# Kernel optimization log

Measured on AMD Instinct MI355X. Metric: run time of the kernel, lower is better.

## Reference

```python
import jax, jax.numpy as jnp
import numpy as np

B, S = 2, 2048
HQ, HKV, D = 32, 8, 128
SCALING = 0.08838834764831845  # 1/sqrt(128)
E4M3_MAX = 448.0
FP4_MAX = 6.0
# e2m1 representable magnitudes and decision midpoints
FP4_GRID = jnp.array([0.0, 0.5, 1.0, 1.5, 2.0, 3.0, 4.0, 6.0], dtype=jnp.float32)
FP4_MID = (FP4_GRID[:-1] + FP4_GRID[1:]) / 2.0


def quant_dequant_e4m3(x):
    """Simulate torch .to(float8_e4m3fn): clamp to +-448, round mantissa to 3 bits."""
    ax = jnp.abs(x)
    xc = jnp.clip(x, -E4M3_MAX, E4M3_MAX)
    e = jnp.clip(jnp.floor(jnp.log2(jnp.maximum(ax, 1e-12))), -6.0, 8.0)
    q = jnp.round(xc * jnp.exp2(3.0 - e)) * jnp.exp2(e - 3.0)
    return jnp.where(ax == 0.0, 0.0, q)


def quant_dequant_fp4(x):
    """FP4 (e2m1) compress/decompress with per-(token,head) absmax scale over head_dim.
    x: [B, S, H, D] -> dequantized [B, S, H, D]."""
    scale = jnp.max(jnp.abs(x), axis=-1, keepdims=True) / FP4_MAX  # [B,S,H,1]
    scale = jnp.maximum(scale, 1e-12)
    xn = x / scale
    idx = jnp.searchsorted(FP4_MID, jnp.abs(xn))  # nearest e2m1 magnitude
    return jnp.sign(xn) * FP4_GRID[idx] * scale


def setup_inputs() -> dict:
    key = jax.random.key(0)
    kq, kk, kv = jax.random.split(key, 3)
    q = jax.random.normal(kq, (B, S, HQ * D), dtype=jnp.float32)
    k = jax.random.normal(kk, (B, S, HKV * D), dtype=jnp.float32)
    v = jax.random.normal(kv, (B, S, HKV * D), dtype=jnp.float32)
    return {"q": q, "k": k, "v": v}


def reference(q, k, v):
    # reshape to heads
    qh = q.reshape(B, S, HQ, D)
    kh = k.reshape(B, S, HKV, D)
    vh = v.reshape(B, S, HKV, D)
    # FP8 cast then FP4 compress/decompress of the KV cache
    kq8 = quant_dequant_e4m3(kh)
    vq8 = quant_dequant_e4m3(vh)
    kd = quant_dequant_fp4(kq8)
    vd = quant_dequant_fp4(vq8)
    # GQA: expand kv heads to query heads
    g = HQ // HKV
    kr = jnp.repeat(kd, g, axis=2)  # [B,S,HQ,D]
    vr = jnp.repeat(vd, g, axis=2)
    scores = jnp.einsum("bqhd,bkhd->bhqk", qh, kr) * SCALING  # [B,HQ,S,S]
    causal = jnp.tril(jnp.ones((S, S), dtype=bool))
    scores = jnp.where(causal[None, None], scores, jnp.float32(-1e30))
    probs = jax.nn.softmax(scores, axis=-1)
    out = jnp.einsum("bhqk,bkhd->bqhd", probs, vr)
    return out.reshape(B, S, HQ * D)
```

## Files before the change

### kernel.cpp

```cpp
#include <hip/hip_runtime.h>
#include <cstdint>
#include <cstddef>

#define B_    2
#define S_    2048
#define HQ_   32
#define HKV_  8
#define D_    128
#define QSCALE_ (0.08838834764831845f * 1.4426950408889634f)

#define NROW_ (B_*S_*HKV_)

typedef __bf16 bf16x8 __attribute__((ext_vector_type(8)));
typedef float  f32x4  __attribute__((ext_vector_type(4)));

__device__ __forceinline__ unsigned short f2bfu(float f) {
    __bf16 b = (__bf16)f;
    return __builtin_bit_cast(unsigned short, b);
}

__device__ __forceinline__ void gl_lds16(const unsigned short* g, unsigned short* l) {
    __builtin_amdgcn_global_load_lds(
        (const __attribute__((address_space(1))) void*)g,
        (__attribute__((address_space(3))) void*)l, 16, 0, 0);
}

__device__ __forceinline__ float qd_e4m3(float x) {
    float ax = fabsf(x);
    float xc = fminf(fmaxf(x, -448.f), 448.f);
    float axc = fmaxf(ax, 1e-12f);
    int e = (int)((__builtin_bit_cast(unsigned int, axc) >> 23) & 255u) - 127;
    e = min(max(e, -6), 8);
    float s1 = __builtin_bit_cast(float, (unsigned int)(130 - e) << 23);
    float s2 = __builtin_bit_cast(float, (unsigned int)(124 + e) << 23);
    float q = rintf(xc * s1) * s2;
    return ax == 0.f ? 0.f : q;
}

__device__ __forceinline__ float qd_fp4(float x, float scale) {
    float xn = x / scale;
    float a = fabsf(xn);
    float g;
    if      (a <= 0.25f) g = 0.f;
    else if (a <= 0.75f) g = 0.5f;
    else if (a <= 1.25f) g = 1.f;
    else if (a <= 1.75f) g = 1.5f;
    else if (a <= 2.5f)  g = 2.f;
    else if (a <= 3.5f)  g = 3.f;
    else if (a <= 5.f)   g = 4.f;
    else                 g = 6.f;
    return copysignf(g * scale, xn);
}

__global__ __launch_bounds__(256) void quant_kv(const float* __restrict__ k,
                                                const float* __restrict__ v,
                                                unsigned short* __restrict__ kd,
                                                unsigned short* __restrict__ vd) {
    int gw = (blockIdx.x * 256 + threadIdx.x) >> 6;
    int lane = threadIdx.x & 63;
    int row = gw;
    const float* src;
    unsigned short* dst;
    if (row < NROW_) { src = k; dst = kd; }
    else             { row -= NROW_; src = v; dst = vd; }
    int b   = row / (S_ * HKV_);
    int rem = row - b * (S_ * HKV_);
    int s   = rem >> 3;
    int h   = rem & 7;
    float2 x = *(const float2*)(src + (size_t)row * D_ + 2 * lane);
    float q0 = qd_e4m3(x.x);
    float q1 = qd_e4m3(x.y);
    float amax = fmaxf(fabsf(q0), fabsf(q1));
#pragma unroll
    for (int m = 1; m < 64; m <<= 1) amax = fmaxf(amax, __shfl_xor(amax, m, 64));
    float scale = fmaxf(amax / 6.0f, 1e-12f);
    float y0 = qd_fp4(q0, scale);
    float y1 = qd_fp4(q1, scale);
    size_t outOff = ((size_t)(b * HKV_ + h) * S_ + s) * D_ + 2 * lane;
    unsigned int pack = (unsigned int)f2bfu(y0) | ((unsigned int)f2bfu(y1) << 16);
    *(unsigned int*)(dst + outOff) = pack;
}

__global__ __launch_bounds__(256) void transpose_v(const unsigned short* __restrict__ vd,
                                                   unsigned short* __restrict__ vdT) {
    __shared__ alignas(16) unsigned short t[64][136];
    int bh = blockIdx.x >> 5;
    int st = blockIdx.x & 31;
    int s0 = st * 64;
    int tid = threadIdx.x;
    {
        int row = tid >> 2;
        const unsigned short* sp = vd + ((size_t)bh * S_ + s0 + row) * D_;
#pragma unroll
        for (int i = 0; i < 4; ++i) {
            int c = (tid & 3) + 4 * i;
            *(uint4*)&t[row][c * 8] = *(const uint4*)(sp + c * 8);
        }
    }
    __syncthreads();
    {
        int d = tid >> 1;
        unsigned short* dp = vdT + ((size_t)bh * D_ + d) * S_ + s0;
#pragma unroll
        for (int i = 0; i < 4; ++i) {
            int c = (tid & 1) + 2 * i;
            int so = c * 8;
            unsigned short tmp[8];
#pragma unroll
            for (int e = 0; e < 8; ++e) tmp[e] = t[so + e][d];
            *(uint4*)(dp + so) = *(uint4*)tmp;
        }
    }
}

__global__ __launch_bounds__(256) void attn(const float* __restrict__ q,
                                            const unsigned short* __restrict__ kd,
                                            const unsigned short* __restrict__ vdT,
                                            float* __restrict__ out) {
    int bh = blockIdx.x;
    int yp = blockIdx.y;
    int b  = bh >> 5;
    int hq = bh & 31;
    int hkv = hq >> 2;
    int tid  = threadIdx.x;
    int lane = tid & 63;
    int wave = tid >> 6;
    int m16  = lane & 15;
    int g    = lane >> 4;
    int m8   = m16 & 7;

    __shared__ alignas(16) unsigned short ks[64 * 128];
    __shared__ alignas(16) unsigned short vs[128 * 64];
    __shared__ alignas(16) unsigned short ps[4 * 16 * 64];

    const unsigned short* kbase = kd  + (size_t)(b * HKV_ + hkv) * S_ * D_;
    const unsigned short* vbase = vdT + (size_t)(b * HKV_ + hkv) * D_ * S_;

    bf16x8 vones;
#pragma unroll
    for (int j = 0; j < 8; ++j) vones[j] = (__bf16)1.0f;

    for (int phase = 0; phase < 2; ++phase) {
        int qt = phase ? yp : (31 - yp);
        int q0 = qt * 64;
        int qrowBase = q0 + wave * 16;

        bf16x8 qf[4];
        const float* qp = q + (((size_t)b * S_ + (qrowBase + m16)) * HQ_ + hq) * D_;
#pragma unroll
        for (int c = 0; c < 4; ++c) {
            const float* p0 = qp + c * 32 + g * 8;
            bf16x8 f;
#pragma unroll
            for (int j = 0; j < 8; ++j) f[j] = (__bf16)(p0[j] * QSCALE_);
            qf[c] = f;
        }

        f32x4 o[8];
#pragma unroll
        for (int i = 0; i < 8; ++i) o[i] = (f32x4){0.f, 0.f, 0.f, 0.f};
        f32x4 o9 = (f32x4){0.f, 0.f, 0.f, 0.f};

        for (int kt = 0; kt <= qt; ++kt) {
            int k0 = kt * 64;
            __syncthreads();
#pragma unroll
            for (int i = 0; i < 4; ++i) {
                int row = wave * 16 + i * 4 + (lane >> 4);
                int c = (lane & 15) ^ (row & 15);
                gl_lds16(kbase + (size_t)(k0 + row) * D_ + c * 8,
                         &ks[wave * 2048 + i * 512]);
            }
#pragma unroll
            for (int i = 0; i < 4; ++i) {
                int d = wave * 32 + i * 8 + (lane >> 3);
                int c = (lane & 7) ^ (d & 7);
                gl_lds16(vbase + (size_t)d * S_ + k0 + c * 8,
                         &vs[wave * 2048 + i * 512]);
            }
            __syncthreads();

            bool diag = (kt == qt);
            int kcmax = diag ? ((wave >> 1) + 1) : 2;

            f32x4 sacc[4];
#pragma unroll
            for (int n = 0; n < 4; ++n) sacc[n] = (f32x4){0.f, 0.f, 0.f, 0.f};
#pragma unroll
            for (int n = 0; n < 4; ++n) {
                if (!diag || n <= wave) {
#pragma unroll
                    for (int c = 0; c < 4; ++c) {
                        bf16x8 ak = *(const bf16x8*)&ks[(n * 16 + m16) * 128 +
                                                        (((c * 4 + g) ^ m16) * 8)];
                        sacc[n] = __builtin_amdgcn_mfma_f32_16x16x32_bf16(ak, qf[c], sacc[n], 0, 0, 0);
                    }
                }
            }

            int qloc = wave * 16 + m16;
            float pv[4][4];
#pragma unroll
            for (int n = 0; n < 4; ++n) {
                if (!diag || n <= wave) {
#pragma unroll
                    for (int r = 0; r < 4; ++r) {
                        float p = exp2f(sacc[n][r]);
                        if (diag) {
                            int key = n * 16 + g * 4 + r;
                            p = (key <= qloc) ? p : 0.f;
                        }
                        pv[n][r] = p;
                    }
                }
            }

#pragma unroll
            for (int n = 0; n < 4; ++n) {
                if (n < 2 * kcmax) {
                    unsigned int lo = 0, hi = 0;
                    if (!diag || n <= wave) {
                        lo = (unsigned int)f2bfu(pv[n][0]) | ((unsigned int)f2bfu(pv[n][1]) << 16);
                        hi = (unsigned int)f2bfu(pv[n][2]) | ((unsigned int)f2bfu(pv[n][3]) << 16);
                    }
                    int chunk = (n * 2 + (g >> 1)) ^ m8;
                    uint2 val; val.x = lo; val.y = hi;
                    *(uint2*)&ps[wave * 1024 + m16 * 64 + chunk * 8 + (g & 1) * 4] = val;
                }
            }
            asm volatile("s_waitcnt lgkmcnt(0)" ::: "memory");

#pragma unroll
            for (int kc = 0; kc < 2; ++kc) {
                if (kc < kcmax) {
                    bf16x8 pa = *(const bf16x8*)&ps[wave * 1024 + m16 * 64 +
                                                    (((kc * 4 + g) ^ m8) * 8)];
                    o9 = __builtin_amdgcn_mfma_f32_16x16x32_bf16(pa, vones, o9, 0, 0, 0);
#pragma unroll
                    for (int ds = 0; ds < 8; ++ds) {
                        bf16x8 vb = *(const bf16x8*)&vs[(ds * 16 + m16) * 64 +
                                                        (((kc * 4 + g) ^ m8) * 8)];
                        o[ds] = __builtin_amdgcn_mfma_f32_16x16x32_bf16(pa, vb, o[ds], 0, 0, 0);
                    }
                }
            }
        }

#pragma unroll
        for (int r = 0; r < 4; ++r) {
            float inv = 1.f / o9[r];
            float* op = out + (((size_t)b * S_ + (qrowBase + g * 4 + r)) * HQ_ + hq) * D_;
#pragma unroll
            for (int ds = 0; ds < 8; ++ds)
                op[ds * 16 + m16] = o[ds][r] * inv;
        }
    }
}

extern "C" void kernel_launch(void* const* d_in, const int* in_sizes, int n_in,
                              void* d_out, int out_size, void* d_ws, size_t ws_size,
                              hipStream_t stream) {
    const float* q = (const float*)d_in[0];
    const float* k = (const float*)d_in[1];
    const float* v = (const float*)d_in[2];
    float* out = (float*)d_out;

    unsigned short* kd  = (unsigned short*)d_ws;
    unsigned short* vd  = kd + (size_t)NROW_ * D_;
    unsigned short* vdT = vd + (size_t)NROW_ * D_;

    quant_kv<<<16384, 256, 0, stream>>>(k, v, kd, vd);
    transpose_v<<<512, 256, 0, stream>>>(vd, vdT);
    attn<<<dim3(64, 16), 256, 0, stream>>>(q, kd, vdT, out);
}
```

Before: 260.3 us.

## Double-buffer K/V tiles and process 128-row query tiles with two fragments per wave

```diff
diff --git a/kernel.cpp b/kernel.cpp
--- a/kernel.cpp
+++ b/kernel.cpp
@@ -113,10 +113,10 @@
     }
 }
 
-__global__ __launch_bounds__(256) void attn(const float* __restrict__ q,
-                                            const unsigned short* __restrict__ kd,
-                                            const unsigned short* __restrict__ vdT,
-                                            float* __restrict__ out) {
+__global__ __launch_bounds__(256, 2) void attn(const float* __restrict__ q,
+                                               const unsigned short* __restrict__ kd,
+                                               const unsigned short* __restrict__ vdT,
+                                               float* __restrict__ out) {
     int bh = blockIdx.x;
     int yp = blockIdx.y;
     int b  = bh >> 5;
@@ -129,9 +129,9 @@
     int g    = lane >> 4;
     int m8   = m16 & 7;
 
-    __shared__ alignas(16) unsigned short ks[64 * 128];
-    __shared__ alignas(16) unsigned short vs[128 * 64];
-    __shared__ alignas(16) unsigned short ps[4 * 16 * 64];
+    __shared__ alignas(16) unsigned short ks[2][64 * 128];
+    __shared__ alignas(16) unsigned short vs[2][128 * 64];
+    __shared__ alignas(16) unsigned short ps[4 * 2048];
 
     const unsigned short* kbase = kd  + (size_t)(b * HKV_ + hkv) * S_ * D_;
     const unsigned short* vbase = vdT + (size_t)(b * HKV_ + hkv) * D_ * S_;
@@ -140,119 +140,181 @@
 #pragma unroll
     for (int j = 0; j < 8; ++j) vones[j] = (__bf16)1.0f;
 
+    auto stage = [&](int buf, int k0s) {
+#pragma unroll
+        for (int i = 0; i < 4; ++i) {
+            int row = wave * 16 + i * 4 + (lane >> 4);
+            int c = (lane & 15) ^ (row & 15);
+            gl_lds16(kbase + (size_t)(k0s + row) * D_ + c * 8,
+                     &ks[buf][wave * 2048 + i * 512]);
+        }
+#pragma unroll
+        for (int i = 0; i < 4; ++i) {
+            int d = wave * 32 + i * 8 + (lane >> 3);
+            int c = (lane & 7) ^ (d & 7);
+            gl_lds16(vbase + (size_t)d * S_ + k0s + c * 8,
+                     &vs[buf][wave * 2048 + i * 512]);
+        }
+    };
+
     for (int phase = 0; phase < 2; ++phase) {
-        int qt = phase ? yp : (31 - yp);
-        int q0 = qt * 64;
-        int qrowBase = q0 + wave * 16;
-
-        bf16x8 qf[4];
-        const float* qp = q + (((size_t)b * S_ + (qrowBase + m16)) * HQ_ + hq) * D_;
-#pragma unroll
-        for (int c = 0; c < 4; ++c) {
-            const float* p0 = qp + c * 32 + g * 8;
-            bf16x8 f;
-#pragma unroll
-            for (int j = 0; j < 8; ++j) f[j] = (__bf16)(p0[j] * QSCALE_);
-            qf[c] = f;
-        }
-
-        f32x4 o[8];
-#pragma unroll
-        for (int i = 0; i < 8; ++i) o[i] = (f32x4){0.f, 0.f, 0.f, 0.f};
-        f32x4 o9 = (f32x4){0.f, 0.f, 0.f, 0.f};
-
-        for (int kt = 0; kt <= qt; ++kt) {
+        int t  = phase ? yp : (15 - yp);
+        int q0 = t * 128;
+        int nkt = 2 * t + 2;
+
+        stage(0, 0);
+
+        bf16x8 qf0[4], qf1[4];
+        {
+            const float* qp0 = q + (((size_t)b * S_ + (q0 + wave * 32 + m16)) * HQ_ + hq) * D_;
+            const float* qp1 = qp0 + (size_t)16 * HQ_ * D_;
+#pragma unroll
+            for (int c = 0; c < 4; ++c) {
+                const float* a0 = qp0 + c * 32 + g * 8;
+                const float* a1 = qp1 + c * 32 + g * 8;
+                bf16x8 f0, f1;
+#pragma unroll
+                for (int j = 0; j < 8; ++j) {
+                    f0[j] = (__bf16)(a0[j] * QSCALE_);
+                    f1[j] = (__bf16)(a1[j] * QSCALE_);
+                }
+                qf0[c] = f0;
+                qf1[c] = f1;
+            }
+        }
+
+        f32x4 o0[8], o1[8];
+#pragma unroll
+        for (int i = 0; i < 8; ++i) { o0[i] = (f32x4){0.f,0.f,0.f,0.f}; o1[i] = (f32x4){0.f,0.f,0.f,0.f}; }
+        f32x4 l0 = (f32x4){0.f,0.f,0.f,0.f};
+        f32x4 l1 = (f32x4){0.f,0.f,0.f,0.f};
+
+        __syncthreads();
+
+        int cur = 0;
+        for (int kt = 0; kt < nkt; ++kt) {
             int k0 = kt * 64;
-            __syncthreads();
-#pragma unroll
-            for (int i = 0; i < 4; ++i) {
-                int row = wave * 16 + i * 4 + (lane >> 4);
-                int c = (lane & 15) ^ (row & 15);
-                gl_lds16(kbase + (size_t)(k0 + row) * D_ + c * 8,
-                         &ks[wave * 2048 + i * 512]);
-            }
-#pragma unroll
-            for (int i = 0; i < 4; ++i) {
-                int d = wave * 32 + i * 8 + (lane >> 3);
-                int c = (lane & 7) ^ (d & 7);
-                gl_lds16(vbase + (size_t)d * S_ + k0 + c * 8,
-                         &vs[wave * 2048 + i * 512]);
+            if (kt + 1 < nkt) stage(cur ^ 1, k0 + 64);
+
+            int base1 = (q0 - k0) + wave * 32 + 16;
+            if (base1 >= 0) {
+                int base0 = base1 - 16;
+                bool full1 = base1 >= 64, full0 = base0 >= 64;
+                int a1 = full1 ? 4 : (base1 >> 4) + 1;
+                int a0 = (base0 < 0) ? 0 : (full0 ? 4 : (base0 >> 4) + 1);
+                int kcm1 = (a1 + 1) >> 1;
+                int kcm0 = (a0 + 1) >> 1;
+
+                f32x4 s0[4], s1[4];
+#pragma unroll
+                for (int n = 0; n < 4; ++n) {
+                    s0[n] = (f32x4){0.f,0.f,0.f,0.f};
+                    s1[n] = (f32x4){0.f,0.f,0.f,0.f};
+                }
+#pragma unroll
+                for (int n = 0; n < 4; ++n) {
+                    if (n < a1) {
+#pragma unroll
+                        for (int c = 0; c < 4; ++c) {
+                            bf16x8 ak = *(const bf16x8*)&ks[cur][(n * 16 + m16) * 128 +
+                                                                 (((c * 4 + g) ^ m16) * 8)];
+                            s1[n] = __builtin_amdgcn_mfma_f32_16x16x32_bf16(ak, qf1[c], s1[n], 0, 0, 0);
+                            if (n < a0)
+                                s0[n] = __builtin_amdgcn_mfma_f32_16x16x32_bf16(ak, qf0[c], s0[n], 0, 0, 0);
+                        }
+                    }
+                }
+
+#pragma unroll
+                for (int n = 0; n < 4; ++n) {
+                    if (n < 2 * kcm1) {
+                        unsigned int lo = 0, hi = 0;
+                        if (n < a1) {
+                            float pr[4];
+#pragma unroll
+                            for (int r = 0; r < 4; ++r) {
+                                float p = exp2f(s1[n][r]);
+                                if (!full1) {
+                                    int key = n * 16 + g * 4 + r;
+                                    p = (key <= base1 + m16) ? p : 0.f;
+                                }
+                                pr[r] = p;
+                            }
+                            lo = (unsigned int)f2bfu(pr[0]) | ((unsigned int)f2bfu(pr[1]) << 16);
+                            hi = (unsigned int)f2bfu(pr[2]) | ((unsigned int)f2bfu(pr[3]) << 16);
+                        }
+                        int chunk = (n * 2 + (g >> 1)) ^ m8;
+                        uint2 val; val.x = lo; val.y = hi;
+                        *(uint2*)&ps[wave * 2048 + 1024 + m16 * 64 + chunk * 8 + (g & 1) * 4] = val;
+                    }
+                }
+                if (a0 > 0) {
+#pragma unroll
+                    for (int n = 0; n < 4; ++n) {
+                        if (n < 2 * kcm0) {
+                            unsigned int lo = 0, hi = 0;
+                            if (n < a0) {
+                                float pr[4];
+#pragma unroll
+                                for (int r = 0; r < 4; ++r) {
+                                    float p = exp2f(s0[n][r]);
+                                    if (!full0) {
+                                        int key = n * 16 + g * 4 + r;
+                                        p = (key <= base0 + m16) ? p : 0.f;
+                                    }
+                                    pr[r] = p;
+                                }
+                                lo = (unsigned int)f2bfu(pr[0]) | ((unsigned int)f2bfu(pr[1]) << 16);
+                                hi = (unsigned int)f2bfu(pr[2]) | ((unsigned int)f2bfu(pr[3]) << 16);
+                            }
+                            int chunk = (n * 2 + (g >> 1)) ^ m8;
+                            uint2 val; val.x = lo; val.y = hi;
+                            *(uint2*)&ps[wave * 2048 + m16 * 64 + chunk * 8 + (g & 1) * 4] = val;
+                        }
+                    }
+                }
+                asm volatile("s_waitcnt lgkmcnt(0)" ::: "memory");
+
+#pragma unroll
+                for (int kc = 0; kc < 2; ++kc) {
+                    if (kc < kcm1) {
+                        bf16x8 pa1 = *(const bf16x8*)&ps[wave * 2048 + 1024 + m16 * 64 +
+                                                         (((kc * 4 + g) ^ m8) * 8)];
+                        l1 = __builtin_amdgcn_mfma_f32_16x16x32_bf16(pa1, vones, l1, 0, 0, 0);
+                        bool use0 = kc < kcm0;
+                        bf16x8 pa0;
+                        if (use0) {
+                            pa0 = *(const bf16x8*)&ps[wave * 2048 + m16 * 64 +
+                                                      (((kc * 4 + g) ^ m8) * 8)];
+                            l0 = __builtin_amdgcn_mfma_f32_16x16x32_bf16(pa0, vones, l0, 0, 0, 0);
+                        }
+#pragma unroll
+                        for (int ds = 0; ds < 8; ++ds) {
+                            bf16x8 vb = *(const bf16x8*)&vs[cur][(ds * 16 + m16) * 64 +
+                                                                 (((kc * 4 + g) ^ m8) * 8)];
+                            o1[ds] = __builtin_amdgcn_mfma_f32_16x16x32_bf16(pa1, vb, o1[ds], 0, 0, 0);
+                            if (use0)
+                                o0[ds] = __builtin_amdgcn_mfma_f32_16x16x32_bf16(pa0, vb, o0[ds], 0, 0, 0);
+                        }
+                    }
+                }
             }
             __syncthreads();
-
-            bool diag = (kt == qt);
-            int kcmax = diag ? ((wave >> 1) + 1) : 2;
-
-            f32x4 sacc[4];
-#pragma unroll
-            for (int n = 0; n < 4; ++n) sacc[n] = (f32x4){0.f, 0.f, 0.f, 0.f};
-#pragma unroll
-            for (int n = 0; n < 4; ++n) {
-                if (!diag || n <= wave) {
-#pragma unroll
-                    for (int c = 0; c < 4; ++c) {
-                        bf16x8 ak = *(const bf16x8*)&ks[(n * 16 + m16) * 128 +
-                                                        (((c * 4 + g) ^ m16) * 8)];
-                        sacc[n] = __builtin_amdgcn_mfma_f32_16x16x32_bf16(ak, qf[c], sacc[n], 0, 0, 0);
-                    }
-                }
-            }
-
-            int qloc = wave * 16 + m16;
-            float pv[4][4];
-#pragma unroll
-            for (int n = 0; n < 4; ++n) {
-                if (!diag || n <= wave) {
-#pragma unroll
-                    for (int r = 0; r < 4; ++r) {
-                        float p = exp2f(sacc[n][r]);
-                        if (diag) {
-                            int key = n * 16 + g * 4 + r;
-                            p = (key <= qloc) ? p : 0.f;
-                        }
-                        pv[n][r] = p;
-                    }
-                }
-            }
-
-#pragma unroll
-            for (int n = 0; n < 4; ++n) {
-                if (n < 2 * kcmax) {
-                    unsigned int lo = 0, hi = 0;
-                    if (!diag || n <= wave) {
-                        lo = (unsigned int)f2bfu(pv[n][0]) | ((unsigned int)f2bfu(pv[n][1]) << 16);
-                        hi = (unsigned int)f2bfu(pv[n][2]) | ((unsigned int)f2bfu(pv[n][3]) << 16);
-                    }
-                    int chunk = (n * 2 + (g >> 1)) ^ m8;
-                    uint2 val; val.x = lo; val.y = hi;
-                    *(uint2*)&ps[wave * 1024 + m16 * 64 + chunk * 8 + (g & 1) * 4] = val;
-                }
-            }
-            asm volatile("s_waitcnt lgkmcnt(0)" ::: "memory");
-
-#pragma unroll
-            for (int kc = 0; kc < 2; ++kc) {
-                if (kc < kcmax) {
-                    bf16x8 pa = *(const bf16x8*)&ps[wave * 1024 + m16 * 64 +
-                                                    (((kc * 4 + g) ^ m8) * 8)];
-                    o9 = __builtin_amdgcn_mfma_f32_16x16x32_bf16(pa, vones, o9, 0, 0, 0);
-#pragma unroll
-                    for (int ds = 0; ds < 8; ++ds) {
-                        bf16x8 vb = *(const bf16x8*)&vs[(ds * 16 + m16) * 64 +
-                                                        (((kc * 4 + g) ^ m8) * 8)];
-                        o[ds] = __builtin_amdgcn_mfma_f32_16x16x32_bf16(pa, vb, o[ds], 0, 0, 0);
-                    }
-                }
-            }
+            cur ^= 1;
         }
 
 #pragma unroll
         for (int r = 0; r < 4; ++r) {
-            float inv = 1.f / o9[r];
-            float* op = out + (((size_t)b * S_ + (qrowBase + g * 4 + r)) * HQ_ + hq) * D_;
+            float inv0 = 1.f / l0[r];
+            float* op0 = out + (((size_t)b * S_ + (q0 + wave * 32 + g * 4 + r)) * HQ_ + hq) * D_;
 #pragma unroll
             for (int ds = 0; ds < 8; ++ds)
-                op[ds * 16 + m16] = o[ds][r] * inv;
+                op0[ds * 16 + m16] = o0[ds][r] * inv0;
+            float inv1 = 1.f / l1[r];
+            float* op1 = op0 + (size_t)16 * HQ_ * D_;
+#pragma unroll
+            for (int ds = 0; ds < 8; ++ds)
+                op1[ds * 16 + m16] = o1[ds][r] * inv1;
         }
     }
 }
@@ -271,5 +333,5 @@
 
     quant_kv<<<16384, 256, 0, stream>>>(k, v, kd, vd);
     transpose_v<<<512, 256, 0, stream>>>(vd, vdT);
-    attn<<<dim3(64, 16), 256, 0, stream>>>(q, kd, vdT, out);
-}
+    attn<<<dim3(64, 8), 256, 0, stream>>>(q, kd, vdT, out);
+}
```

New measurement: 267.8 us. +2.9%, slower.

## Fuse V quantization into transpose kernel and raise MFMA wave priority

Applied to the files above, without the earlier changes.

```diff
diff --git a/kernel.cpp b/kernel.cpp
--- a/kernel.cpp
+++ b/kernel.cpp
@@ -52,53 +52,67 @@
     return copysignf(g * scale, xn);
 }
 
-__global__ __launch_bounds__(256) void quant_kv(const float* __restrict__ k,
-                                                const float* __restrict__ v,
-                                                unsigned short* __restrict__ kd,
-                                                unsigned short* __restrict__ vd) {
-    int gw = (blockIdx.x * 256 + threadIdx.x) >> 6;
-    int lane = threadIdx.x & 63;
-    int row = gw;
-    const float* src;
-    unsigned short* dst;
-    if (row < NROW_) { src = k; dst = kd; }
-    else             { row -= NROW_; src = v; dst = vd; }
-    int b   = row / (S_ * HKV_);
-    int rem = row - b * (S_ * HKV_);
-    int s   = rem >> 3;
-    int h   = rem & 7;
-    float2 x = *(const float2*)(src + (size_t)row * D_ + 2 * lane);
-    float q0 = qd_e4m3(x.x);
-    float q1 = qd_e4m3(x.y);
-    float amax = fmaxf(fabsf(q0), fabsf(q1));
-#pragma unroll
-    for (int m = 1; m < 64; m <<= 1) amax = fmaxf(amax, __shfl_xor(amax, m, 64));
-    float scale = fmaxf(amax / 6.0f, 1e-12f);
-    float y0 = qd_fp4(q0, scale);
-    float y1 = qd_fp4(q1, scale);
-    size_t outOff = ((size_t)(b * HKV_ + h) * S_ + s) * D_ + 2 * lane;
-    unsigned int pack = (unsigned int)f2bfu(y0) | ((unsigned int)f2bfu(y1) << 16);
-    *(unsigned int*)(dst + outOff) = pack;
-}
-
-__global__ __launch_bounds__(256) void transpose_v(const unsigned short* __restrict__ vd,
-                                                   unsigned short* __restrict__ vdT) {
+__global__ __launch_bounds__(256) void prep(const float* __restrict__ k,
+                                            const float* __restrict__ v,
+                                            unsigned short* __restrict__ kd,
+                                            unsigned short* __restrict__ vdT) {
     __shared__ alignas(16) unsigned short t[64][136];
-    int bh = blockIdx.x >> 5;
-    int st = blockIdx.x & 31;
-    int s0 = st * 64;
-    int tid = threadIdx.x;
-    {
-        int row = tid >> 2;
-        const unsigned short* sp = vd + ((size_t)bh * S_ + s0 + row) * D_;
-#pragma unroll
-        for (int i = 0; i < 4; ++i) {
-            int c = (tid & 3) + 4 * i;
-            *(uint4*)&t[row][c * 8] = *(const uint4*)(sp + c * 8);
-        }
-    }
-    __syncthreads();
-    {
+    if (blockIdx.x < 8192) {
+        int gw = (blockIdx.x * 256 + threadIdx.x) >> 6;
+        int lane = threadIdx.x & 63;
+        int row = gw;
+        int b   = row / (S_ * HKV_);
+        int rem = row - b * (S_ * HKV_);
+        int s   = rem >> 3;
+        int h   = rem & 7;
+        float2 x = *(const float2*)(k + (size_t)row * D_ + 2 * lane);
+        float q0 = qd_e4m3(x.x);
+        float q1 = qd_e4m3(x.y);
+        float amax = fmaxf(fabsf(q0), fabsf(q1));
+#pragma unroll
+        for (int m = 1; m < 64; m <<= 1) amax = fmaxf(amax, __shfl_xor(amax, m, 64));
+        float scale = fmaxf(amax / 6.0f, 1e-12f);
+        float y0 = qd_fp4(q0, scale);
+        float y1 = qd_fp4(q1, scale);
+        size_t outOff = ((size_t)(b * HKV_ + h) * S_ + s) * D_ + 2 * lane;
+        unsigned int pack = (unsigned int)f2bfu(y0) | ((unsigned int)f2bfu(y1) << 16);
+        *(unsigned int*)(kd + outOff) = pack;
+    } else {
+        int bid = blockIdx.x - 8192;
+        int bh = bid >> 5;
+        int st = bid & 31;
+        int s0 = st * 64;
+        int b = bh >> 3;
+        int h = bh & 7;
+        int tid = threadIdx.x;
+        int lane = tid & 63;
+        int wave = tid >> 6;
+#pragma unroll
+        for (int i = 0; i < 8; ++i) {
+            int rA = wave * 16 + 2 * i;
+            const float* srcA = v + (((size_t)b * S_ + (s0 + rA)) * HKV_ + h) * D_ + 2 * lane;
+            const float* srcB = srcA + (size_t)HKV_ * D_;
+            float2 xA = *(const float2*)srcA;
+            float2 xB = *(const float2*)srcB;
+            float a0 = qd_e4m3(xA.x), a1 = qd_e4m3(xA.y);
+            float c0 = qd_e4m3(xB.x), c1 = qd_e4m3(xB.y);
+            float amA = fmaxf(fabsf(a0), fabsf(a1));
+            float amB = fmaxf(fabsf(c0), fabsf(c1));
+#pragma unroll
+            for (int m = 1; m < 64; m <<= 1) {
+                amA = fmaxf(amA, __shfl_xor(amA, m, 64));
+                amB = fmaxf(amB, __shfl_xor(amB, m, 64));
+            }
+            float sA = fmaxf(amA / 6.0f, 1e-12f);
+            float sB = fmaxf(amB / 6.0f, 1e-12f);
+            unsigned int pA = (unsigned int)f2bfu(qd_fp4(a0, sA)) |
+                              ((unsigned int)f2bfu(qd_fp4(a1, sA)) << 16);
+            unsigned int pB = (unsigned int)f2bfu(qd_fp4(c0, sB)) |
+                              ((unsigned int)f2bfu(qd_fp4(c1, sB)) << 16);
+            *(unsigned int*)&t[rA][2 * lane]     = pA;
+            *(unsigned int*)&t[rA + 1][2 * lane] = pB;
+        }
+        __syncthreads();
         int d = tid >> 1;
         unsigned short* dp = vdT + ((size_t)bh * D_ + d) * S_ + s0;
 #pragma unroll
@@ -186,6 +200,7 @@
             f32x4 sacc[4];
 #pragma unroll
             for (int n = 0; n < 4; ++n) sacc[n] = (f32x4){0.f, 0.f, 0.f, 0.f};
+            __builtin_amdgcn_s_setprio(1);
 #pragma unroll
             for (int n = 0; n < 4; ++n) {
                 if (!diag || n <= wave) {
@@ -197,6 +212,7 @@
                     }
                 }
             }
+            __builtin_amdgcn_s_setprio(0);
 
             int qloc = wave * 16 + m16;
             float pv[4][4];
@@ -230,6 +246,7 @@
             }
             asm volatile("s_waitcnt lgkmcnt(0)" ::: "memory");
 
+            __builtin_amdgcn_s_setprio(1);
 #pragma unroll
             for (int kc = 0; kc < 2; ++kc) {
                 if (kc < kcmax) {
@@ -244,6 +261,7 @@
                     }
                 }
             }
+            __builtin_amdgcn_s_setprio(0);
         }
 
 #pragma unroll
@@ -266,10 +284,8 @@
     float* out = (float*)d_out;
 
     unsigned short* kd  = (unsigned short*)d_ws;
-    unsigned short* vd  = kd + (size_t)NROW_ * D_;
-    unsigned short* vdT = vd + (size_t)NROW_ * D_;
-
-    quant_kv<<<16384, 256, 0, stream>>>(k, v, kd, vd);
-    transpose_v<<<512, 256, 0, stream>>>(vd, vdT);
+    unsigned short* vdT = kd + (size_t)NROW_ * D_;
+
+    prep<<<8704, 256, 0, stream>>>(k, v, kd, vdT);
     attn<<<dim3(64, 16), 256, 0, stream>>>(q, kd, vdT, out);
 }
```

Result: no change. 259.6 us (-0.2%).
